# Kernel optimization log

Measured on AMD Instinct MI355X. Metric: run time of the kernel, lower is better.

## Reference

```python
import jax, jax.numpy as jnp
import numpy as np

T_SEQ = 120
BATCH = 256
HID = 512
D_LAG = 32
D_COV = 32
D_OUT = 1
N_LAYERS = 2
D_IN0 = D_LAG + D_COV
BN_EPS = 1e-5
SCALE_EPS = 1e-6
GAMMA = 1.0


def _gru_layer(x, Wih, Whh, bih, bhh):
    # x: [B, T, D] -> [B, T, H]; PyTorch GRU gate order (r, z, n)
    H = Whh.shape[1]
    gx = jnp.einsum('btd,gd->btg', x, Wih) + bih  # [B, T, 3H]
    gx_t = jnp.swapaxes(gx, 0, 1)                 # [T, B, 3H]
    h0 = jnp.zeros((x.shape[0], H), x.dtype)

    def step(h, g):
        gh = h @ Whh.T + bhh
        r = jax.nn.sigmoid(g[:, :H] + gh[:, :H])
        z = jax.nn.sigmoid(g[:, H:2 * H] + gh[:, H:2 * H])
        n = jnp.tanh(g[:, 2 * H:] + r * gh[:, 2 * H:])
        h = (1.0 - z) * n + z * h
        return h, h

    _, hs = jax.lax.scan(step, h0, gx_t)
    return jnp.swapaxes(hs, 0, 1)  # [B, T, H]


def setup_inputs() -> dict:
    key = jax.random.key(0)
    ks = jax.random.split(key, 16)
    s = 1.0 / np.sqrt(HID)
    inp = {
        'X_emb': jnp.zeros((T_SEQ, BATCH, 1), dtype=jnp.int32),
        'X_cov': jax.random.normal(ks[0], (T_SEQ, BATCH, D_COV), dtype=jnp.float32),
        'X_lag': jax.random.normal(ks[1], (T_SEQ, BATCH, D_LAG), dtype=jnp.float32),
        'y': jax.random.normal(ks[2], (T_SEQ, BATCH, D_OUT), dtype=jnp.float32),
        'd_outputseqlen': 24,
        'len_win': 30,
        'W_ih0': jax.random.uniform(ks[3], (3 * HID, D_IN0), minval=-s, maxval=s),
        'W_hh0': jax.random.uniform(ks[4], (3 * HID, HID), minval=-s, maxval=s),
        'b_ih0': jax.random.uniform(ks[5], (3 * HID,), minval=-s, maxval=s),
        'b_hh0': jax.random.uniform(ks[6], (3 * HID,), minval=-s, maxval=s),
        'W_ih1': jax.random.uniform(ks[7], (3 * HID, HID), minval=-s, maxval=s),
        'W_hh1': jax.random.uniform(ks[8], (3 * HID, HID), minval=-s, maxval=s),
        'b_ih1': jax.random.uniform(ks[9], (3 * HID,), minval=-s, maxval=s),
        'b_hh1': jax.random.uniform(ks[10], (3 * HID,), minval=-s, maxval=s),
        'gate_W': jax.random.normal(ks[11], (N_LAYERS, T_SEQ, T_SEQ * 2 * HID)) * 0.05,
        'gate_b': jnp.zeros((N_LAYERS, T_SEQ)),
        'bn_gamma': jnp.ones((N_LAYERS, T_SEQ)),
        'bn_beta': jnp.zeros((N_LAYERS, T_SEQ)),
        'fc_W': jax.random.uniform(ks[12], (D_OUT, HID), minval=-s, maxval=s),
        'fc_b': jnp.zeros((D_OUT,)),
    }
    return inp


def reference(X_emb, X_cov, X_lag, y, d_outputseqlen, len_win,
              W_ih0, W_hh0, b_ih0, b_hh0, W_ih1, W_hh1, b_ih1, b_hh1,
              gate_W, gate_b, bn_gamma, bn_beta, fc_W, fc_b):
    T, B, _ = X_lag.shape
    half = B // 2
    x = jnp.concatenate([X_lag, X_cov], axis=-1)   # [T, B, D]
    x = jnp.transpose(x, (1, 0, 2))                # [B, T, D]

    gru_params = [(W_ih0, W_hh0, b_ih0, b_hh0), (W_ih1, W_hh1, b_ih1, b_hh1)]
    outs = []
    gate_weights = []
    for l, (Wih, Whh, bih, bhh) in enumerate(gru_params):
        x = _gru_layer(x, Wih, Whh, bih, bhh)      # [B, T, H]
        outs.append(x)
        # process_gate_weight: src/tgt halves concatenated on feature dim
        x_all = jnp.concatenate([x[:half], x[half:]], axis=2).reshape(half, -1)  # [B/2, T*2H]
        z = x_all @ gate_W[l].T + gate_b[l]        # [B/2, T]
        m = z.mean(axis=0)
        v = ((z - m) ** 2).mean(axis=0)            # biased var (BatchNorm training mode)
        w = jax.nn.sigmoid(bn_gamma[l] * (z - m) / jnp.sqrt(v + BN_EPS) + bn_beta[l])
        gate_weights.append(jax.nn.softmax(w.mean(axis=0)))  # [T]

    # prediction head (original uses fc_scale for both loc and scale)
    fea = outs[-1]
    lin = fea[:, -d_outputseqlen:, :] @ fc_W.T + fc_b          # [B, L, D_OUT]
    y_hat_loc = jnp.transpose(lin, (1, 0, 2))                  # [L, B, D_OUT]
    y_hat_scale = jnp.transpose(jax.nn.softplus(lin), (1, 0, 2)) + SCALE_EPS
    y_t = y[-d_outputseqlen:]
    log_prob = (-0.5 * ((y_t - y_hat_loc) / y_hat_scale) ** 2
                - jnp.log(y_hat_scale) - 0.5 * jnp.log(2.0 * jnp.pi))
    loss_y = -log_prob.mean()

    # linear-MMD transfer loss over windowed (j, k) pairs, all layers
    idx = jnp.arange(T)
    mask = (jnp.abs(idx[:, None] - idx[None, :]) <= len_win).astype(fea.dtype)  # [T, T]
    loss_transfer = jnp.zeros(())
    for l, o in enumerate(outs):
        ms = o[:half].mean(axis=0)   # [T, H]
        mt = o[half:].mean(axis=0)   # [T, H]
        # D[j,k] = ||ms[j]-mt[k]||^2 == linear MMD of columns j (src) and k (tgt)
        D = ((ms ** 2).sum(-1)[:, None] + (mt ** 2).sum(-1)[None, :]
             - 2.0 * ms @ mt.T)
        loss_transfer = loss_transfer + jnp.dot(gate_weights[l], (mask * D).sum(axis=1))
    total_loss = loss_y + GAMMA * loss_transfer
    return (total_loss, loss_y, y_hat_loc, y_hat_scale, jnp.stack(gate_weights))
```

## Files before the change

kernel.cpp:

```cpp
#include <hip/hip_runtime.h>
#include <math.h>

#define T_SEQ 120
#define BATCH 256
#define HID   512
#define G3    1536
#define MROWS (BATCH*T_SEQ)
#define TS    (T_SEQ*HID)
#define KGATE 122880
#define FSTRIDE 16

typedef __attribute__((ext_vector_type(8))) short bf16x8;
typedef __attribute__((ext_vector_type(4))) float f32x4;

__device__ __forceinline__ unsigned short f2bf(float f) {
    union { float f; unsigned u; } x; x.f = f;
    unsigned r = x.u + 0x7fffu + ((x.u >> 16) & 1u);
    return (unsigned short)(r >> 16);
}
__device__ __forceinline__ float bf2f(unsigned short u) {
    union { unsigned u; float f; } x; x.u = ((unsigned)u) << 16; return x.f;
}
__device__ __forceinline__ float sigm_fast(float x) {
    return 1.f / (1.f + __expf(-x));
}
__device__ __forceinline__ float tanh_fast(float x) {
    float e = __expf(2.f * x);
    return 1.f - 2.f / (e + 1.f);
}

__global__ void build_x(const float* __restrict__ X_lag,
                        const float* __restrict__ X_cov,
                        float* __restrict__ x_in)
{
    int idx = blockIdx.x * 256 + threadIdx.x;
    int d = idx & 63;
    int m = idx >> 6;
    int b = m / 120, t = m - b * 120;
    float v;
    if (d < 32) v = X_lag[((size_t)t * BATCH + b) * 32 + d];
    else        v = X_cov[((size_t)t * BATCH + b) * 32 + (d - 32)];
    x_in[idx] = v;
}

__global__ void cast_whh0(const float* __restrict__ W, unsigned short* __restrict__ o)
{
    int i = blockIdx.x * 256 + threadIdx.x;
    o[i] = f2bf(W[i]);
}

__global__ void cast_wcat1(const float* __restrict__ Whh, const float* __restrict__ Wih,
                           unsigned short* __restrict__ o)
{
    int i = blockIdx.x * 256 + threadIdx.x;
    int row = i >> 10, c = i & 1023;
    float v = (c < 512) ? Whh[row * 512 + c] : Wih[row * 512 + (c - 512)];
    o[i] = f2bf(v);
}

__global__ void mkbias(const float* __restrict__ bih0, const float* __restrict__ bhh0,
                       const float* __restrict__ bih1, const float* __restrict__ bhh1,
                       float* __restrict__ bcomb0, float* __restrict__ bc1)
{
    int n = blockIdx.x * 256 + threadIdx.x;
    bcomb0[n] = bih0[n] + (n < 1024 ? bhh0[n] : 0.f);
    bc1[n]    = bih1[n] + (n < 1024 ? bhh1[n] : 0.f);
}

__global__ __launch_bounds__(256) void gemm_abt_t(
    const float* __restrict__ A, const float* __restrict__ B,
    const float* __restrict__ bias, unsigned short* __restrict__ C,
    int M, int N, int K)
{
    __shared__ float As[32][129];
    __shared__ float Bs[32][129];
    int m0 = blockIdx.x * 128;
    int n0 = blockIdx.y * 128;
    int tid = threadIdx.x;
    int tx = tid & 15, ty = tid >> 4;
    float acc[8][8] = {};
    for (int k0 = 0; k0 < K; k0 += 32) {
        #pragma unroll
        for (int i = 0; i < 16; i++) {
            int e = tid + i * 256;
            int row = e >> 5, col = e & 31;
            As[col][row] = A[(size_t)(m0 + row) * K + k0 + col];
            Bs[col][row] = B[(size_t)(n0 + row) * K + k0 + col];
        }
        __syncthreads();
        #pragma unroll
        for (int kk = 0; kk < 32; kk++) {
            float a[8], b[8];
            #pragma unroll
            for (int i = 0; i < 8; i++) a[i] = As[kk][ty + i * 16];
            #pragma unroll
            for (int j = 0; j < 8; j++) b[j] = Bs[kk][tx + j * 16];
            #pragma unroll
            for (int i = 0; i < 8; i++)
                #pragma unroll
                for (int j = 0; j < 8; j++) acc[i][j] += a[i] * b[j];
        }
        __syncthreads();
    }
    #pragma unroll
    for (int i = 0; i < 8; i++) {
        int m = m0 + ty + i * 16;
        int b = m / 120, t = m - b * 120;
        #pragma unroll
        for (int j = 0; j < 8; j++) {
            int n = n0 + tx + j * 16;
            C[((size_t)t * 256 + b) * G3 + n] = f2bf(acc[i][j] + bias[n]);
        }
    }
}

__device__ __forceinline__ bool wait16(const int* __restrict__ fb, int thr, int lane)
{
    const int* ap = fb + (lane & 15) * FSTRIDE;
    for (int it = 0; it < 100000; ++it) {
        int v = __hip_atomic_load(ap, __ATOMIC_RELAXED, __HIP_MEMORY_SCOPE_AGENT);
        if (__all(v >= thr)) return true;
        __builtin_amdgcn_s_sleep(1);
    }
    return false;
}

__global__ __launch_bounds__(256) void gru_xcd(
    const unsigned short* __restrict__ gx0,
    const unsigned short* __restrict__ Whh0,
    const unsigned short* __restrict__ Wcat1,
    const float* __restrict__ bhh0,
    const float* __restrict__ bc1,
    const float* __restrict__ bhh1,
    unsigned short* __restrict__ out0,
    unsigned short* __restrict__ out1,
    int* __restrict__ flags,
    int* __restrict__ rolecnt)
{
    __shared__ unsigned short wlds[96 * 520];
    __shared__ int role_s;

    int xcd;
    asm("s_getreg_b32 %0, hwreg(20, 0, 32)" : "=s"(xcd));
    xcd &= 7;
    if (threadIdx.x == 0) role_s = atomicAdd(&rolecnt[xcd * 16], 1);
    __syncthreads();
    const int role = role_s;
    if (role >= 32) return;

    const int layer = role >> 4;
    const int jb    = role & 15;
    const int j0    = jb * 32;
    const int tid   = threadIdx.x;
    const int w     = tid >> 6, lane = tid & 63;
    const int l15   = lane & 15, l4 = lane >> 4;
    const int jt    = w & 1, bt = w >> 1;
    const int jloc  = jt * 16 + l15;
    const int j     = j0 + jloc;
    const int bloc0 = bt * 16;
    const int bg0   = xcd * 32;

    {
        const unsigned short* Wsrc = layer ? Wcat1 : Whh0;
        const int wstr = layer ? 1024 : 512;
        for (int c = tid; c < 96 * 64; c += 256) {
            int lr = c >> 6, ck = c & 63;
            int grow = (lr >> 5) * 512 + j0 + (lr & 31);
            bf16x8 v = *(const bf16x8*)(Wsrc + (size_t)grow * wstr + ck * 8);
            *(bf16x8*)&wlds[lr * 520 + ck * 8] = v;
        }
    }
    float bn_, br_ = 0.f, bz_ = 0.f, bnx_ = 0.f;
    if (layer) { br_ = bc1[j]; bz_ = bc1[512 + j]; bnx_ = bc1[1024 + j]; bn_ = bhh1[1024 + j]; }
    else       { bn_ = bhh0[1024 + j]; }
    float carry[4] = {0.f, 0.f, 0.f, 0.f};

    const int* f0b = flags + (0 * 8 + xcd) * 16 * FSTRIDE;
    const int* f1b = flags + (1 * 8 + xcd) * 16 * FSTRIDE;
    int* myf = flags + ((layer * 8 + xcd) * 16 + jb) * FSTRIDE;
    __syncthreads();

    if (!layer) {
        for (int t = 0; t < T_SEQ; t++) {
            unsigned short gr_[4], gz_[4], gn_[4];
            #pragma unroll
            for (int rr = 0; rr < 4; rr++) {
                int b = bg0 + bloc0 + 4 * l4 + rr;
                const unsigned short* gp = gx0 + ((size_t)t * 256 + b) * G3 + j;
                gr_[rr] = gp[0]; gz_[rr] = gp[512]; gn_[rr] = gp[1024];
            }
            asm volatile("" ::: "memory");

            if (!wait16(f0b, t - 1, lane)) break;

            f32x4 a0 = {0,0,0,0}, a1 = {0,0,0,0}, a2 = {0,0,0,0};
            if (t > 0) {
                bf16x8 Areg[16];
                #pragma unroll
                for (int ks = 0; ks < 16; ks++)
                    Areg[ks] = *(const bf16x8*)(out0 + ((size_t)(bg0 + bloc0 + l15) * T_SEQ + (t - 1)) * 512 + ks * 32 + 8 * l4);
                #pragma unroll
                for (int ks = 0; ks < 16; ks++) {
                    const int ko = ks * 32 + 8 * l4;
                    bf16x8 B0 = *(const bf16x8*)&wlds[(0 * 32 + jloc) * 520 + ko];
                    bf16x8 B1 = *(const bf16x8*)&wlds[(1 * 32 + jloc) * 520 + ko];
                    bf16x8 B2 = *(const bf16x8*)&wlds[(2 * 32 + jloc) * 520 + ko];
                    a0 = __builtin_amdgcn_mfma_f32_16x16x32_bf16(Areg[ks], B0, a0, 0, 0, 0);
                    a1 = __builtin_amdgcn_mfma_f32_16x16x32_bf16(Areg[ks], B1, a1, 0, 0, 0);
                    a2 = __builtin_amdgcn_mfma_f32_16x16x32_bf16(Areg[ks], B2, a2, 0, 0, 0);
                }
            }
            #pragma unroll
            for (int rr = 0; rr < 4; rr++) {
                int b = bg0 + bloc0 + 4 * l4 + rr;
                float r = sigm_fast(bf2f(gr_[rr]) + a0[rr]);
                float z = sigm_fast(bf2f(gz_[rr]) + a1[rr]);
                float n = tanh_fast(bf2f(gn_[rr]) + r * (a2[rr] + bn_));
                float h = (1.f - z) * n + z * carry[rr];
                carry[rr] = h;
                out0[((size_t)b * T_SEQ + t) * 512 + j] = f2bf(h);
            }
            asm volatile("s_waitcnt vmcnt(0)" ::: "memory");
            __syncthreads();
            if (tid == 0)
                __hip_atomic_store(myf, t, __ATOMIC_RELAXED, __HIP_MEMORY_SCOPE_AGENT);
        }
    } else {
        for (int t = 0; t < T_SEQ; t++) {
            f32x4 a0 = {0,0,0,0}, a1 = {0,0,0,0}, a2 = {0,0,0,0}, a3 = {0,0,0,0};
            if (!wait16(f1b, t - 1, lane)) break;
            if (t > 0) {
                bf16x8 Areg[16];
                #pragma unroll
                for (int ks = 0; ks < 16; ks++)
                    Areg[ks] = *(const bf16x8*)(out1 + ((size_t)(bg0 + bloc0 + l15) * T_SEQ + (t - 1)) * 512 + ks * 32 + 8 * l4);
                #pragma unroll
                for (int ks = 0; ks < 16; ks++) {
                    const int ko = ks * 32 + 8 * l4;
                    bf16x8 B0 = *(const bf16x8*)&wlds[(0 * 32 + jloc) * 520 + ko];
                    bf16x8 B1 = *(const bf16x8*)&wlds[(1 * 32 + jloc) * 520 + ko];
                    bf16x8 B2 = *(const bf16x8*)&wlds[(2 * 32 + jloc) * 520 + ko];
                    a0 = __builtin_amdgcn_mfma_f32_16x16x32_bf16(Areg[ks], B0, a0, 0, 0, 0);
                    a1 = __builtin_amdgcn_mfma_f32_16x16x32_bf16(Areg[ks], B1, a1, 0, 0, 0);
                    a2 = __builtin_amdgcn_mfma_f32_16x16x32_bf16(Areg[ks], B2, a2, 0, 0, 0);
                }
            }
            if (!wait16(f0b, t, lane)) break;
            {
                bf16x8 Areg[16];
                #pragma unroll
                for (int ks = 0; ks < 16; ks++)
                    Areg[ks] = *(const bf16x8*)(out0 + ((size_t)(bg0 + bloc0 + l15) * T_SEQ + t) * 512 + ks * 32 + 8 * l4);
                #pragma unroll
                for (int ks = 0; ks < 16; ks++) {
                    const int ko = ks * 32 + 8 * l4;
                    const unsigned short* wb = Wcat1 + (size_t)j * 1024 + 512 + ko;
                    bf16x8 B0 = *(const bf16x8*)(wb);
                    bf16x8 B1 = *(const bf16x8*)(wb + 512 * 1024);
                    bf16x8 B2 = *(const bf16x8*)(wb + 1024 * 1024);
                    a0 = __builtin_amdgcn_mfma_f32_16x16x32_bf16(Areg[ks], B0, a0, 0, 0, 0);
                    a1 = __builtin_amdgcn_mfma_f32_16x16x32_bf16(Areg[ks], B1, a1, 0, 0, 0);
                    a3 = __builtin_amdgcn_mfma_f32_16x16x32_bf16(Areg[ks], B2, a3, 0, 0, 0);
                }
            }
            #pragma unroll
            for (int rr = 0; rr < 4; rr++) {
                int b = bg0 + bloc0 + 4 * l4 + rr;
                float r = sigm_fast(a0[rr] + br_);
                float z = sigm_fast(a1[rr] + bz_);
                float n = tanh_fast(a3[rr] + bnx_ + r * (a2[rr] + bn_));
                float h = (1.f - z) * n + z * carry[rr];
                carry[rr] = h;
                out1[((size_t)b * T_SEQ + t) * 512 + j] = f2bf(h);
            }
            asm volatile("s_waitcnt vmcnt(0)" ::: "memory");
            __syncthreads();
            if (tid == 0)
                __hip_atomic_store(myf, t, __ATOMIC_RELAXED, __HIP_MEMORY_SCOPE_AGENT);
        }
    }
}

__global__ __launch_bounds__(256) void zpart_kernel(
    const unsigned short* __restrict__ out, const float* __restrict__ Gw,
    float* __restrict__ zp)
{
    __shared__ float Os[128][33];
    __shared__ float Gs[128][33];
    int bk = blockIdx.x;
    int t = bk >> 3, half = (bk >> 2) & 1, cq = bk & 3;
    int tid = threadIdx.x;
    int tx = tid & 15, ty = tid >> 4;
    float acc[8][8] = {};
    int cbase = cq * 128;
    for (int c0 = cbase; c0 < cbase + 128; c0 += 32) {
        #pragma unroll
        for (int i = 0; i < 16; i++) {
            int e = tid + i * 256;
            int row = e >> 5, col = e & 31;
            Os[row][col] = bf2f(out[((size_t)(row + half * 128) * T_SEQ + t) * 512 + c0 + col]);
            float v = 0.f;
            if (row < 120)
                v = Gw[(size_t)row * KGATE + (size_t)t * 1024 + half * 512 + c0 + col];
            Gs[row][col] = v;
        }
        __syncthreads();
        #pragma unroll
        for (int kk = 0; kk < 32; kk++) {
            float a[8], g[8];
            #pragma unroll
            for (int i = 0; i < 8; i++) a[i] = Os[ty + i * 16][kk];
            #pragma unroll
            for (int j = 0; j < 8; j++) g[j] = Gs[tx + j * 16][kk];
            #pragma unroll
            for (int i = 0; i < 8; i++)
                #pragma unroll
                for (int j = 0; j < 8; j++) acc[i][j] += a[i] * g[j];
        }
        __syncthreads();
    }
    float* zb = zp + (size_t)bk * (128 * 120);
    #pragma unroll
    for (int i = 0; i < 8; i++) {
        int ii = ty + i * 16;
        #pragma unroll
        for (int j = 0; j < 8; j++) {
            int r = tx + j * 16;
            if (r < 120) zb[ii * 120 + r] = acc[i][j];
        }
    }
}

__global__ void zreduce(const float* __restrict__ zp,
                        const float* __restrict__ gate_b_l,
                        float* __restrict__ z)
{
    int idx = blockIdx.x * 256 + threadIdx.x;
    if (idx >= 128 * 120) return;
    float s = 0.f;
    for (int c = 0; c < 960; c++) s += zp[(size_t)c * (128 * 120) + idx];
    z[idx] = s + gate_b_l[idx % 120];
}

__global__ __launch_bounds__(128) void bn_col(
    const float* __restrict__ z, const float* __restrict__ gamma,
    const float* __restrict__ beta, float* __restrict__ wm)
{
    int r = blockIdx.x, i = threadIdx.x;
    __shared__ float sh[2];
    float v = z[i * 120 + r];
    float s = v;
    for (int o = 32; o > 0; o >>= 1) s += __shfl_down(s, o);
    if ((i & 63) == 0) sh[i >> 6] = s;
    __syncthreads();
    float m = (sh[0] + sh[1]) * (1.f / 128.f);
    __syncthreads();
    float d = (v - m) * (v - m);
    for (int o = 32; o > 0; o >>= 1) d += __shfl_down(d, o);
    if ((i & 63) == 0) sh[i >> 6] = d;
    __syncthreads();
    float var = (sh[0] + sh[1]) * (1.f / 128.f);
    float w = 1.f / (1.f + expf(-(gamma[r] * (v - m) / sqrtf(var + 1e-5f) + beta[r])));
    __syncthreads();
    float ws_ = w;
    for (int o = 32; o > 0; o >>= 1) ws_ += __shfl_down(ws_, o);
    if ((i & 63) == 0) sh[i >> 6] = ws_;
    __syncthreads();
    if (i == 0) wm[r] = (sh[0] + sh[1]) * (1.f / 128.f);
}

__global__ __launch_bounds__(128) void softmax120(
    const float* __restrict__ wm, float* __restrict__ g_out,
    float* __restrict__ g_ws)
{
    int i = threadIdx.x;
    __shared__ float sh[2];
    float v = (i < 120) ? wm[i] : -1e30f;
    float m = v;
    for (int o = 32; o > 0; o >>= 1) m = fmaxf(m, __shfl_down(m, o));
    if ((i & 63) == 0) sh[i >> 6] = m;
    __syncthreads();
    float mx = fmaxf(sh[0], sh[1]);
    float e = (i < 120) ? expf(v - mx) : 0.f;
    __syncthreads();
    float se = e;
    for (int o = 32; o > 0; o >>= 1) se += __shfl_down(se, o);
    if ((i & 63) == 0) sh[i >> 6] = se;
    __syncthreads();
    float sum = sh[0] + sh[1];
    if (i < 120) { float g = e / sum; g_out[i] = g; g_ws[i] = g; }
}

__global__ void halfmeans(const unsigned short* __restrict__ out,
                          float* __restrict__ ms, float* __restrict__ mt)
{
    int idx = blockIdx.x * 256 + threadIdx.x;
    int half = idx >= TS;
    int tc = idx - half * TS;
    const unsigned short* base = out + (size_t)(half * 128) * TS + tc;
    float s = 0.f;
    for (int i = 0; i < 128; i++) s += bf2f(base[(size_t)i * TS]);
    s *= (1.f / 128.f);
    if (half) mt[tc] = s; else ms[tc] = s;
}

__global__ __launch_bounds__(512) void transfer_part(
    const float* __restrict__ ms, const float* __restrict__ mt,
    const float* __restrict__ gw, const int* __restrict__ lenw,
    float* __restrict__ part)
{
    int t = blockIdx.x, c = threadIdx.x;
    int lw = lenw[0];
    int j0 = t - lw; if (j0 < 0) j0 = 0;
    int j1 = t + lw; if (j1 > 119) j1 = 119;
    float m_c = ms[(size_t)t * 512 + c];
    float acc = 0.f;
    for (int j = j0; j <= j1; j++) {
        float d = m_c - mt[(size_t)j * 512 + c];
        acc += d * d;
    }
    for (int o = 32; o > 0; o >>= 1) acc += __shfl_down(acc, o);
    __shared__ float sh[8];
    if ((c & 63) == 0) sh[c >> 6] = acc;
    __syncthreads();
    if (c == 0) {
        float s = 0.f;
        #pragma unroll
        for (int k = 0; k < 8; k++) s += sh[k];
        part[t] = gw[t] * s;
    }
}

__global__ __launch_bounds__(256) void yhat_kernel(
    const unsigned short* __restrict__ out1, const float* __restrict__ y,
    const float* __restrict__ fcW, const float* __restrict__ fcb,
    int dsl, float* __restrict__ dout, float* __restrict__ lp_rows)
{
    int wid = blockIdx.x * 4 + (threadIdx.x >> 6);
    int lane = threadIdx.x & 63;
    int tt = wid >> 8, b = wid & 255;
    int t = T_SEQ - dsl + tt;
    const unsigned short* row = out1 + ((size_t)b * T_SEQ + t) * 512;
    float s = 0.f;
    #pragma unroll
    for (int k = 0; k < 8; k++) s += bf2f(row[lane + 64 * k]) * fcW[lane + 64 * k];
    for (int o = 32; o > 0; o >>= 1) s += __shfl_down(s, o);
    if (lane == 0) {
        float loc = s + fcb[0];
        float sp = fmaxf(loc, 0.f) + log1pf(expf(-fabsf(loc)));
        float scale = sp + 1e-6f;
        dout[2 + tt * 256 + b] = loc;
        dout[2 + dsl * 256 + tt * 256 + b] = scale;
        float yt = y[(size_t)t * 256 + b];
        float u = (yt - loc) / scale;
        lp_rows[wid] = -0.5f * u * u - logf(scale) - 0.91893853320467274f;
    }
}

__global__ __launch_bounds__(64) void finalize(
    const float* __restrict__ lp_rows, const float* __restrict__ part0,
    const float* __restrict__ part1, float* __restrict__ dout, int n_lp)
{
    int i = threadIdx.x;
    float s = 0.f;
    for (int k = i; k < n_lp; k += 64) s += lp_rows[k];
    for (int o = 32; o > 0; o >>= 1) s += __shfl_down(s, o);
    float tr = 0.f;
    for (int k = i; k < 120; k += 64) tr += part0[k] + part1[k];
    for (int o = 32; o > 0; o >>= 1) tr += __shfl_down(tr, o);
    if (i == 0) {
        float ly = -s / (float)n_lp;
        dout[1] = ly;
        dout[0] = ly + tr;
    }
}

extern "C" void kernel_launch(void* const* d_in, const int* in_sizes, int n_in,
                              void* d_out, int out_size, void* d_ws, size_t ws_size,
                              hipStream_t stream)
{
    const float* X_cov  = (const float*)d_in[1];
    const float* X_lag  = (const float*)d_in[2];
    const float* y      = (const float*)d_in[3];
    const int*   lenw   = (const int*)d_in[5];
    const float* W_ih0  = (const float*)d_in[6];
    const float* W_hh0  = (const float*)d_in[7];
    const float* b_ih0  = (const float*)d_in[8];
    const float* b_hh0  = (const float*)d_in[9];
    const float* W_ih1  = (const float*)d_in[10];
    const float* W_hh1  = (const float*)d_in[11];
    const float* b_ih1  = (const float*)d_in[12];
    const float* b_hh1  = (const float*)d_in[13];
    const float* gate_W = (const float*)d_in[14];
    const float* gate_b = (const float*)d_in[15];
    const float* bn_g   = (const float*)d_in[16];
    const float* bn_b   = (const float*)d_in[17];
    const float* fc_W   = (const float*)d_in[18];
    const float* fc_b   = (const float*)d_in[19];
    float* dout = (float*)d_out;
    float* ws   = (float*)d_ws;

    float* x_in    = ws;
    unsigned short* gx0bf = (unsigned short*)(ws + 1966080);
    unsigned short* out0  = (unsigned short*)(ws + 25559040);
    unsigned short* out1  = (unsigned short*)(ws + 33423360);
    unsigned short* Whh0bf  = (unsigned short*)(ws + 41287680);
    unsigned short* Wcat1bf = (unsigned short*)(ws + 41680896);
    float* zmat    = ws + 42467328;
    float* wm      = ws + 42482688;
    float* gw_ws   = ws + 42482808;
    float* msb     = ws + 42483048;
    float* mtb     = ws + 42544488;
    float* part    = ws + 42605928;
    float* bcomb0  = ws + 42606168;
    float* bc1     = ws + 42607704;
    int*   flags   = (int*)(ws + 42609240);
    int*   rolecnt = (int*)(ws + 42613336);
    float* zp      = ws + 1966080;
    float* lp_rows = x_in;

    int dsl = (out_size - 2 - 2 * T_SEQ) / (2 * BATCH);

    build_x<<<dim3(7680), 256, 0, stream>>>(X_lag, X_cov, x_in);
    cast_whh0<<<dim3(3072), 256, 0, stream>>>(W_hh0, Whh0bf);
    cast_wcat1<<<dim3(6144), 256, 0, stream>>>(W_hh1, W_ih1, Wcat1bf);
    mkbias<<<dim3(6), 256, 0, stream>>>(b_ih0, b_hh0, b_ih1, b_hh1, bcomb0, bc1);
    hipMemsetAsync(flags, 0xFF, 4096 * sizeof(int), stream);
    hipMemsetAsync(rolecnt, 0, 128 * sizeof(int), stream);

    gemm_abt_t<<<dim3(240, 12), 256, 0, stream>>>(x_in, W_ih0, bcomb0, gx0bf,
                                                  MROWS, G3, 64);

    gru_xcd<<<dim3(320), 256, 0, stream>>>(gx0bf, Whh0bf, Wcat1bf,
                                           b_hh0, bc1, b_hh1,
                                           out0, out1, flags, rolecnt);

    for (int l = 0; l < 2; l++) {
        const unsigned short* o = l ? out1 : out0;
        zpart_kernel<<<960, 256, 0, stream>>>(o, gate_W + (size_t)l * 120 * KGATE, zp);
        zreduce<<<60, 256, 0, stream>>>(zp, gate_b + l * 120, zmat);
        bn_col<<<120, 128, 0, stream>>>(zmat, bn_g + l * 120, bn_b + l * 120, wm);
        softmax120<<<1, 128, 0, stream>>>(wm, dout + 2 + 2 * dsl * 256 + l * 120,
                                          gw_ws + l * 120);
        halfmeans<<<480, 256, 0, stream>>>(o, msb, mtb);
        transfer_part<<<120, 512, 0, stream>>>(msb, mtb, gw_ws + l * 120, lenw,
                                               part + l * 120);
    }

    yhat_kernel<<<dsl * 64, 256, 0, stream>>>(out1, y, fc_W, fc_b, dsl, dout, lp_rows);
    finalize<<<1, 64, 0, stream>>>(lp_rows, part, part + 120, dout, dsl * 256);
}
```

Measured before the change: 1.893 ms.

## Replace per-block flag barriers with per-wave atomic step counters in GRU

The per-block flag array, where each block waits on 16 flags with a block-wide __syncthreads before publishing, is replaced by one shared counter per layer and XCD. Each wave increments it after its stores and spins on it reaching 64*t. This removes the intra-block barrier and the 16-way flag poll, and waves proceed independently. In exchange, 64 waves contend on a single atomic cache line and the spin has no sleep, which may add memory traffic. Wave-level fetch_add after only a vmcnt wait could also weaken ordering.

```diff
diff --git a/kernel.cpp b/kernel.cpp
--- a/kernel.cpp
+++ b/kernel.cpp
@@ -8,7 +8,7 @@
 #define MROWS (BATCH*T_SEQ)
 #define TS    (T_SEQ*HID)
 #define KGATE 122880
-#define FSTRIDE 16
+#define CSTRIDE 32
 
 typedef __attribute__((ext_vector_type(8))) short bf16x8;
 typedef __attribute__((ext_vector_type(4))) float f32x4;
@@ -114,13 +114,11 @@
     }
 }
 
-__device__ __forceinline__ bool wait16(const int* __restrict__ fb, int thr, int lane)
-{
-    const int* ap = fb + (lane & 15) * FSTRIDE;
-    for (int it = 0; it < 100000; ++it) {
-        int v = __hip_atomic_load(ap, __ATOMIC_RELAXED, __HIP_MEMORY_SCOPE_AGENT);
-        if (__all(v >= thr)) return true;
-        __builtin_amdgcn_s_sleep(1);
+__device__ __forceinline__ bool wave_wait(const int* __restrict__ cnt, int thr)
+{
+    for (int it = 0; it < 2000000; ++it) {
+        int v = __hip_atomic_load(cnt, __ATOMIC_RELAXED, __HIP_MEMORY_SCOPE_AGENT);
+        if (v >= thr) return true;
     }
     return false;
 }
@@ -134,7 +132,7 @@
     const float* __restrict__ bhh1,
     unsigned short* __restrict__ out0,
     unsigned short* __restrict__ out1,
-    int* __restrict__ flags,
+    int* __restrict__ cnts,
     int* __restrict__ rolecnt)
 {
     __shared__ unsigned short wlds[96 * 520];
@@ -175,9 +173,9 @@
     else       { bn_ = bhh0[1024 + j]; }
     float carry[4] = {0.f, 0.f, 0.f, 0.f};
 
-    const int* f0b = flags + (0 * 8 + xcd) * 16 * FSTRIDE;
-    const int* f1b = flags + (1 * 8 + xcd) * 16 * FSTRIDE;
-    int* myf = flags + ((layer * 8 + xcd) * 16 + jb) * FSTRIDE;
+    const int* c0 = cnts + (0 * 8 + xcd) * CSTRIDE;
+    const int* c1 = cnts + (1 * 8 + xcd) * CSTRIDE;
+    int* myc = cnts + ((layer * 8 + xcd)) * CSTRIDE;
     __syncthreads();
 
     if (!layer) {
@@ -191,7 +189,7 @@
             }
             asm volatile("" ::: "memory");
 
-            if (!wait16(f0b, t - 1, lane)) break;
+            if (!wave_wait(c0, 64 * t)) break;
 
             f32x4 a0 = {0,0,0,0}, a1 = {0,0,0,0}, a2 = {0,0,0,0};
             if (t > 0) {
@@ -221,14 +219,14 @@
                 out0[((size_t)b * T_SEQ + t) * 512 + j] = f2bf(h);
             }
             asm volatile("s_waitcnt vmcnt(0)" ::: "memory");
-            __syncthreads();
-            if (tid == 0)
-                __hip_atomic_store(myf, t, __ATOMIC_RELAXED, __HIP_MEMORY_SCOPE_AGENT);
+            if (lane == 0)
+                __hip_atomic_fetch_add(myc, 1, __ATOMIC_RELAXED,
+                                       __HIP_MEMORY_SCOPE_AGENT);
         }
     } else {
         for (int t = 0; t < T_SEQ; t++) {
             f32x4 a0 = {0,0,0,0}, a1 = {0,0,0,0}, a2 = {0,0,0,0}, a3 = {0,0,0,0};
-            if (!wait16(f1b, t - 1, lane)) break;
+            if (!wave_wait(c1, 64 * t)) break;
             if (t > 0) {
                 bf16x8 Areg[16];
                 #pragma unroll
@@ -245,7 +243,7 @@
                     a2 = __builtin_amdgcn_mfma_f32_16x16x32_bf16(Areg[ks], B2, a2, 0, 0, 0);
                 }
             }
-            if (!wait16(f0b, t, lane)) break;
+            if (!wave_wait(c0, 64 * (t + 1))) break;
             {
                 bf16x8 Areg[16];
                 #pragma unroll
@@ -274,9 +272,9 @@
                 out1[((size_t)b * T_SEQ + t) * 512 + j] = f2bf(h);
             }
             asm volatile("s_waitcnt vmcnt(0)" ::: "memory");
-            __syncthreads();
-            if (tid == 0)
-                __hip_atomic_store(myf, t, __ATOMIC_RELAXED, __HIP_MEMORY_SCOPE_AGENT);
+            if (lane == 0)
+                __hip_atomic_fetch_add(myc, 1, __ATOMIC_RELAXED,
+                                       __HIP_MEMORY_SCOPE_AGENT);
         }
     }
 }
@@ -514,7 +512,7 @@
     float* part    = ws + 42605928;
     float* bcomb0  = ws + 42606168;
     float* bc1     = ws + 42607704;
-    int*   flags   = (int*)(ws + 42609240);
+    int*   cnts    = (int*)(ws + 42609240);
     int*   rolecnt = (int*)(ws + 42613336);
     float* zp      = ws + 1966080;
     float* lp_rows = x_in;
@@ -525,7 +523,7 @@
     cast_whh0<<<dim3(3072), 256, 0, stream>>>(W_hh0, Whh0bf);
     cast_wcat1<<<dim3(6144), 256, 0, stream>>>(W_hh1, W_ih1, Wcat1bf);
     mkbias<<<dim3(6), 256, 0, stream>>>(b_ih0, b_hh0, b_ih1, b_hh1, bcomb0, bc1);
-    hipMemsetAsync(flags, 0xFF, 4096 * sizeof(int), stream);
+    hipMemsetAsync(cnts, 0, 16 * CSTRIDE * sizeof(int), stream);
     hipMemsetAsync(rolecnt, 0, 128 * sizeof(int), stream);
 
     gemm_abt_t<<<dim3(240, 12), 256, 0, stream>>>(x_in, W_ih0, bcomb0, gx0bf,
@@ -533,7 +531,7 @@
 
     gru_xcd<<<dim3(320), 256, 0, stream>>>(gx0bf, Whh0bf, Wcat1bf,
                                            b_hh0, bc1, b_hh1,
-                                           out0, out1, flags, rolecnt);
+                                           out0, out1, cnts, rolecnt);
 
     for (int l = 0; l < 2; l++) {
         const unsigned short* o = l ? out1 : out0;
```

After: 2.083 ms. 10.0% more time.

## Switch GRU step sync to per-wave flags and drop block barriers

Applied to the files above, without the earlier changes.

Each wavefront now publishes its own progress flag, so every group tracks 64 flags instead of 16. This removes the __syncthreads before each flag store, and each lane polls one flag. Spin-waits no longer sleep, and layer 1 checks both of its dependencies in a single combined poll instead of two sequential waits. The flag buffer and memset grow to match, and rolecnt moves to a new offset. The intent is lower per-timestep synchronisation latency in the sequential recurrence, at the cost of more polling traffic and busy-spinning.

```diff
diff --git a/kernel.cpp b/kernel.cpp
--- a/kernel.cpp
+++ b/kernel.cpp
@@ -114,13 +114,28 @@
     }
 }
 
-__device__ __forceinline__ bool wait16(const int* __restrict__ fb, int thr, int lane)
-{
-    const int* ap = fb + (lane & 15) * FSTRIDE;
-    for (int it = 0; it < 100000; ++it) {
+__device__ __forceinline__ bool wait64(const int* __restrict__ base, int thr,
+                                       int lane)
+{
+    const int* ap = base + lane * FSTRIDE;
+    for (int it = 0; it < 2000000; ++it) {
         int v = __hip_atomic_load(ap, __ATOMIC_RELAXED, __HIP_MEMORY_SCOPE_AGENT);
         if (__all(v >= thr)) return true;
-        __builtin_amdgcn_s_sleep(1);
+    }
+    return false;
+}
+__device__ __forceinline__ bool wait64x2(const int* __restrict__ b0, int thr0,
+                                         const int* __restrict__ b1, int thr1,
+                                         int lane)
+{
+    const int* a0 = b0 + lane * FSTRIDE;
+    const int* a1 = b1 + lane * FSTRIDE;
+    for (int it = 0; it < 2000000; ++it) {
+        int v0 = __hip_atomic_load(a0, __ATOMIC_RELAXED, __HIP_MEMORY_SCOPE_AGENT);
+        int v1 = __hip_atomic_load(a1, __ATOMIC_RELAXED, __HIP_MEMORY_SCOPE_AGENT);
+        bool ok0 = __all(v0 >= thr0);
+        bool ok1 = __all(v1 >= thr1);
+        if (ok0 && ok1) return true;
     }
     return false;
 }
@@ -175,9 +190,9 @@
     else       { bn_ = bhh0[1024 + j]; }
     float carry[4] = {0.f, 0.f, 0.f, 0.f};
 
-    const int* f0b = flags + (0 * 8 + xcd) * 16 * FSTRIDE;
-    const int* f1b = flags + (1 * 8 + xcd) * 16 * FSTRIDE;
-    int* myf = flags + ((layer * 8 + xcd) * 16 + jb) * FSTRIDE;
+    const int* f0b = flags + (0 * 8 + xcd) * 64 * FSTRIDE;
+    const int* f1b = flags + (1 * 8 + xcd) * 64 * FSTRIDE;
+    int* myf = flags + ((layer * 8 + xcd) * 64 + (jb * 4 + w)) * FSTRIDE;
     __syncthreads();
 
     if (!layer) {
@@ -191,7 +206,7 @@
             }
             asm volatile("" ::: "memory");
 
-            if (!wait16(f0b, t - 1, lane)) break;
+            if (!wait64(f0b, t - 1, lane)) break;
 
             f32x4 a0 = {0,0,0,0}, a1 = {0,0,0,0}, a2 = {0,0,0,0};
             if (t > 0) {
@@ -221,14 +236,14 @@
                 out0[((size_t)b * T_SEQ + t) * 512 + j] = f2bf(h);
             }
             asm volatile("s_waitcnt vmcnt(0)" ::: "memory");
-            __syncthreads();
-            if (tid == 0)
+            if (lane == 0)
                 __hip_atomic_store(myf, t, __ATOMIC_RELAXED, __HIP_MEMORY_SCOPE_AGENT);
         }
     } else {
         for (int t = 0; t < T_SEQ; t++) {
+            if (!wait64x2(f1b, t - 1, f0b, t, lane)) break;
+
             f32x4 a0 = {0,0,0,0}, a1 = {0,0,0,0}, a2 = {0,0,0,0}, a3 = {0,0,0,0};
-            if (!wait16(f1b, t - 1, lane)) break;
             if (t > 0) {
                 bf16x8 Areg[16];
                 #pragma unroll
@@ -245,7 +260,6 @@
                     a2 = __builtin_amdgcn_mfma_f32_16x16x32_bf16(Areg[ks], B2, a2, 0, 0, 0);
                 }
             }
-            if (!wait16(f0b, t, lane)) break;
             {
                 bf16x8 Areg[16];
                 #pragma unroll
@@ -274,8 +288,7 @@
                 out1[((size_t)b * T_SEQ + t) * 512 + j] = f2bf(h);
             }
             asm volatile("s_waitcnt vmcnt(0)" ::: "memory");
-            __syncthreads();
-            if (tid == 0)
+            if (lane == 0)
                 __hip_atomic_store(myf, t, __ATOMIC_RELAXED, __HIP_MEMORY_SCOPE_AGENT);
         }
     }
@@ -515,7 +528,7 @@
     float* bcomb0  = ws + 42606168;
     float* bc1     = ws + 42607704;
     int*   flags   = (int*)(ws + 42609240);
-    int*   rolecnt = (int*)(ws + 42613336);
+    int*   rolecnt = (int*)(ws + 42625624);
     float* zp      = ws + 1966080;
     float* lp_rows = x_in;
 
@@ -525,7 +538,7 @@
     cast_whh0<<<dim3(3072), 256, 0, stream>>>(W_hh0, Whh0bf);
     cast_wcat1<<<dim3(6144), 256, 0, stream>>>(W_hh1, W_ih1, Wcat1bf);
     mkbias<<<dim3(6), 256, 0, stream>>>(b_ih0, b_hh0, b_ih1, b_hh1, bcomb0, bc1);
-    hipMemsetAsync(flags, 0xFF, 4096 * sizeof(int), stream);
+    hipMemsetAsync(flags, 0xFF, 16384 * sizeof(int), stream);
     hipMemsetAsync(rolecnt, 0, 128 * sizeof(int), stream);
 
     gemm_abt_t<<<dim3(240, 12), 256, 0, stream>>>(x_in, W_ih0, bcomb0, gx0bf,
```

Result: slower. 2.058 ms (+8.7%).

## Fuse layer-0 input projection into GRU kernel and busy-spin flag waits

Applied to the files above, without the earlier changes.

Drops the build_x and layer-0 input GEMM kernels. Layer-0 GRU blocks now load their W_ih0 slice into LDS and compute the input gate contributions per timestep from X_lag/X_cov in fp32, before waiting on the previous step's flag, which removes the gx0 bf16 intermediate round-trip. The flag wait loop replaces s_sleep with dummy FMA work so polling reacts faster, and zreduce's serial sum is split into 8 independent accumulators. The trade-off is extra per-step FMA work and global X loads inside the recurrent critical path, plus busier spinning that competes for issue slots.

```diff
diff --git a/kernel.cpp b/kernel.cpp
--- a/kernel.cpp
+++ b/kernel.cpp
@@ -5,7 +5,6 @@
 #define BATCH 256
 #define HID   512
 #define G3    1536
-#define MROWS (BATCH*T_SEQ)
 #define TS    (T_SEQ*HID)
 #define KGATE 122880
 #define FSTRIDE 16
@@ -29,20 +28,6 @@
     return 1.f - 2.f / (e + 1.f);
 }
 
-__global__ void build_x(const float* __restrict__ X_lag,
-                        const float* __restrict__ X_cov,
-                        float* __restrict__ x_in)
-{
-    int idx = blockIdx.x * 256 + threadIdx.x;
-    int d = idx & 63;
-    int m = idx >> 6;
-    int b = m / 120, t = m - b * 120;
-    float v;
-    if (d < 32) v = X_lag[((size_t)t * BATCH + b) * 32 + d];
-    else        v = X_cov[((size_t)t * BATCH + b) * 32 + (d - 32)];
-    x_in[idx] = v;
-}
-
 __global__ void cast_whh0(const float* __restrict__ W, unsigned short* __restrict__ o)
 {
     int i = blockIdx.x * 256 + threadIdx.x;
@@ -67,69 +52,36 @@
     bc1[n]    = bih1[n] + (n < 1024 ? bhh1[n] : 0.f);
 }
 
-__global__ __launch_bounds__(256) void gemm_abt_t(
-    const float* __restrict__ A, const float* __restrict__ B,
-    const float* __restrict__ bias, unsigned short* __restrict__ C,
-    int M, int N, int K)
-{
-    __shared__ float As[32][129];
-    __shared__ float Bs[32][129];
-    int m0 = blockIdx.x * 128;
-    int n0 = blockIdx.y * 128;
-    int tid = threadIdx.x;
-    int tx = tid & 15, ty = tid >> 4;
-    float acc[8][8] = {};
-    for (int k0 = 0; k0 < K; k0 += 32) {
+__device__ __forceinline__ bool wait16(const int* __restrict__ fb, int thr, int lane)
+{
+    const int* ap = fb + (lane & 15) * FSTRIDE;
+    float x0 = (float)lane, x1 = x0 + 1.f, x2 = x0 + 2.f, x3 = x0 + 3.f;
+    for (int it = 0; it < 300000; ++it) {
+        int v = __hip_atomic_load(ap, __ATOMIC_RELAXED, __HIP_MEMORY_SCOPE_AGENT);
+        if (__all(v >= thr)) {
+            asm volatile("" :: "v"(x0), "v"(x1), "v"(x2), "v"(x3));
+            return true;
+        }
         #pragma unroll
-        for (int i = 0; i < 16; i++) {
-            int e = tid + i * 256;
-            int row = e >> 5, col = e & 31;
-            As[col][row] = A[(size_t)(m0 + row) * K + k0 + col];
-            Bs[col][row] = B[(size_t)(n0 + row) * K + k0 + col];
-        }
-        __syncthreads();
-        #pragma unroll
-        for (int kk = 0; kk < 32; kk++) {
-            float a[8], b[8];
-            #pragma unroll
-            for (int i = 0; i < 8; i++) a[i] = As[kk][ty + i * 16];
-            #pragma unroll
-            for (int j = 0; j < 8; j++) b[j] = Bs[kk][tx + j * 16];
-            #pragma unroll
-            for (int i = 0; i < 8; i++)
-                #pragma unroll
-                for (int j = 0; j < 8; j++) acc[i][j] += a[i] * b[j];
-        }
-        __syncthreads();
-    }
-    #pragma unroll
-    for (int i = 0; i < 8; i++) {
-        int m = m0 + ty + i * 16;
-        int b = m / 120, t = m - b * 120;
-        #pragma unroll
-        for (int j = 0; j < 8; j++) {
-            int n = n0 + tx + j * 16;
-            C[((size_t)t * 256 + b) * G3 + n] = f2bf(acc[i][j] + bias[n]);
-        }
-    }
-}
-
-__device__ __forceinline__ bool wait16(const int* __restrict__ fb, int thr, int lane)
-{
-    const int* ap = fb + (lane & 15) * FSTRIDE;
-    for (int it = 0; it < 100000; ++it) {
-        int v = __hip_atomic_load(ap, __ATOMIC_RELAXED, __HIP_MEMORY_SCOPE_AGENT);
-        if (__all(v >= thr)) return true;
-        __builtin_amdgcn_s_sleep(1);
-    }
+        for (int q = 0; q < 12; q++) {
+            x0 = __builtin_fmaf(x0, 1.000001f, 1e-7f);
+            x1 = __builtin_fmaf(x1, 1.000001f, 1e-7f);
+            x2 = __builtin_fmaf(x2, 1.000001f, 1e-7f);
+            x3 = __builtin_fmaf(x3, 1.000001f, 1e-7f);
+        }
+    }
+    asm volatile("" :: "v"(x0), "v"(x1), "v"(x2), "v"(x3));
     return false;
 }
 
 __global__ __launch_bounds__(256) void gru_xcd(
-    const unsigned short* __restrict__ gx0,
+    const float* __restrict__ X_lag,
+    const float* __restrict__ X_cov,
+    const float* __restrict__ Wih0,
     const unsigned short* __restrict__ Whh0,
     const unsigned short* __restrict__ Wcat1,
     const float* __restrict__ bhh0,
+    const float* __restrict__ bcomb0,
     const float* __restrict__ bc1,
     const float* __restrict__ bhh1,
     unsigned short* __restrict__ out0,
@@ -138,6 +90,7 @@
     int* __restrict__ rolecnt)
 {
     __shared__ unsigned short wlds[96 * 520];
+    __shared__ float wih[96 * 68];
     __shared__ int role_s;
 
     int xcd;
@@ -170,9 +123,17 @@
             *(bf16x8*)&wlds[lr * 520 + ck * 8] = v;
         }
     }
+    if (!layer) {
+        for (int c = tid; c < 96 * 16; c += 256) {
+            int row = c >> 4, q = c & 15;
+            int grow = (row >> 5) * 512 + j0 + (row & 31);
+            float4 v = *(const float4*)(Wih0 + (size_t)grow * 64 + q * 4);
+            *(float4*)&wih[row * 68 + q * 4] = v;
+        }
+    }
     float bn_, br_ = 0.f, bz_ = 0.f, bnx_ = 0.f;
     if (layer) { br_ = bc1[j]; bz_ = bc1[512 + j]; bnx_ = bc1[1024 + j]; bn_ = bhh1[1024 + j]; }
-    else       { bn_ = bhh0[1024 + j]; }
+    else       { br_ = bcomb0[j]; bz_ = bcomb0[512 + j]; bnx_ = bcomb0[1024 + j]; bn_ = bhh0[1024 + j]; }
     float carry[4] = {0.f, 0.f, 0.f, 0.f};
 
     const int* f0b = flags + (0 * 8 + xcd) * 16 * FSTRIDE;
@@ -182,14 +143,24 @@
 
     if (!layer) {
         for (int t = 0; t < T_SEQ; t++) {
-            unsigned short gr_[4], gz_[4], gn_[4];
+            float dr[4] = {}, dz[4] = {}, dn[4] = {};
             #pragma unroll
-            for (int rr = 0; rr < 4; rr++) {
-                int b = bg0 + bloc0 + 4 * l4 + rr;
-                const unsigned short* gp = gx0 + ((size_t)t * 256 + b) * G3 + j;
-                gr_[rr] = gp[0]; gz_[rr] = gp[512]; gn_[rr] = gp[1024];
+            for (int kc = 0; kc < 16; kc++) {
+                float4 w0 = *(const float4*)&wih[(0 * 32 + jloc) * 68 + kc * 4];
+                float4 w1 = *(const float4*)&wih[(1 * 32 + jloc) * 68 + kc * 4];
+                float4 w2 = *(const float4*)&wih[(2 * 32 + jloc) * 68 + kc * 4];
+                #pragma unroll
+                for (int rr = 0; rr < 4; rr++) {
+                    int b = bg0 + bloc0 + 4 * l4 + rr;
+                    const float* xr = (kc < 8)
+                        ? X_lag + ((size_t)t * 256 + b) * 32 + kc * 4
+                        : X_cov + ((size_t)t * 256 + b) * 32 + (kc - 8) * 4;
+                    float4 xv = *(const float4*)xr;
+                    dr[rr] += xv.x * w0.x + xv.y * w0.y + xv.z * w0.z + xv.w * w0.w;
+                    dz[rr] += xv.x * w1.x + xv.y * w1.y + xv.z * w1.z + xv.w * w1.w;
+                    dn[rr] += xv.x * w2.x + xv.y * w2.y + xv.z * w2.z + xv.w * w2.w;
+                }
             }
-            asm volatile("" ::: "memory");
 
             if (!wait16(f0b, t - 1, lane)) break;
 
@@ -213,9 +184,9 @@
             #pragma unroll
             for (int rr = 0; rr < 4; rr++) {
                 int b = bg0 + bloc0 + 4 * l4 + rr;
-                float r = sigm_fast(bf2f(gr_[rr]) + a0[rr]);
-                float z = sigm_fast(bf2f(gz_[rr]) + a1[rr]);
-                float n = tanh_fast(bf2f(gn_[rr]) + r * (a2[rr] + bn_));
+                float r = sigm_fast(dr[rr] + br_ + a0[rr]);
+                float z = sigm_fast(dz[rr] + bz_ + a1[rr]);
+                float n = tanh_fast(dn[rr] + bnx_ + r * (a2[rr] + bn_));
                 float h = (1.f - z) * n + z * carry[rr];
                 carry[rr] = h;
                 out0[((size_t)b * T_SEQ + t) * 512 + j] = f2bf(h);
@@ -337,9 +308,19 @@
 {
     int idx = blockIdx.x * 256 + threadIdx.x;
     if (idx >= 128 * 120) return;
-    float s = 0.f;
-    for (int c = 0; c < 960; c++) s += zp[(size_t)c * (128 * 120) + idx];
-    z[idx] = s + gate_b_l[idx % 120];
+    const float* p = zp + idx;
+    float s0 = 0, s1 = 0, s2 = 0, s3 = 0, s4 = 0, s5 = 0, s6 = 0, s7 = 0;
+    for (int c = 0; c < 960; c += 8) {
+        s0 += p[(size_t)(c + 0) * 15360];
+        s1 += p[(size_t)(c + 1) * 15360];
+        s2 += p[(size_t)(c + 2) * 15360];
+        s3 += p[(size_t)(c + 3) * 15360];
+        s4 += p[(size_t)(c + 4) * 15360];
+        s5 += p[(size_t)(c + 5) * 15360];
+        s6 += p[(size_t)(c + 6) * 15360];
+        s7 += p[(size_t)(c + 7) * 15360];
+    }
+    z[idx] = ((s0 + s1) + (s2 + s3)) + ((s4 + s5) + (s6 + s7)) + gate_b_l[idx % 120];
 }
 
 __global__ __launch_bounds__(128) void bn_col(
@@ -500,39 +481,34 @@
     float* dout = (float*)d_out;
     float* ws   = (float*)d_ws;
 
-    float* x_in    = ws;
-    unsigned short* gx0bf = (unsigned short*)(ws + 1966080);
-    unsigned short* out0  = (unsigned short*)(ws + 25559040);
-    unsigned short* out1  = (unsigned short*)(ws + 33423360);
-    unsigned short* Whh0bf  = (unsigned short*)(ws + 41287680);
-    unsigned short* Wcat1bf = (unsigned short*)(ws + 41680896);
-    float* zmat    = ws + 42467328;
-    float* wm      = ws + 42482688;
-    float* gw_ws   = ws + 42482808;
-    float* msb     = ws + 42483048;
-    float* mtb     = ws + 42544488;
-    float* part    = ws + 42605928;
-    float* bcomb0  = ws + 42606168;
-    float* bc1     = ws + 42607704;
-    int*   flags   = (int*)(ws + 42609240);
-    int*   rolecnt = (int*)(ws + 42613336);
-    float* zp      = ws + 1966080;
-    float* lp_rows = x_in;
+    unsigned short* out0  = (unsigned short*)(ws);
+    unsigned short* out1  = (unsigned short*)(ws + 7864320);
+    unsigned short* Whh0bf  = (unsigned short*)(ws + 15728640);
+    unsigned short* Wcat1bf = (unsigned short*)(ws + 16121856);
+    float* zp      = ws + 16908288;
+    float* zmat    = ws + 31653888;
+    float* wm      = ws + 31669248;
+    float* gw_ws   = ws + 31669368;
+    float* msb     = ws + 31669608;
+    float* mtb     = ws + 31731048;
+    float* part    = ws + 31792488;
+    float* bcomb0  = ws + 31792728;
+    float* bc1     = ws + 31794264;
+    int*   flags   = (int*)(ws + 31795800);
+    int*   rolecnt = (int*)(ws + 31799896);
+    float* lp_rows = ws + 31800024;
 
     int dsl = (out_size - 2 - 2 * T_SEQ) / (2 * BATCH);
 
-    build_x<<<dim3(7680), 256, 0, stream>>>(X_lag, X_cov, x_in);
     cast_whh0<<<dim3(3072), 256, 0, stream>>>(W_hh0, Whh0bf);
     cast_wcat1<<<dim3(6144), 256, 0, stream>>>(W_hh1, W_ih1, Wcat1bf);
     mkbias<<<dim3(6), 256, 0, stream>>>(b_ih0, b_hh0, b_ih1, b_hh1, bcomb0, bc1);
     hipMemsetAsync(flags, 0xFF, 4096 * sizeof(int), stream);
     hipMemsetAsync(rolecnt, 0, 128 * sizeof(int), stream);
 
-    gemm_abt_t<<<dim3(240, 12), 256, 0, stream>>>(x_in, W_ih0, bcomb0, gx0bf,
-                                                  MROWS, G3, 64);
-
-    gru_xcd<<<dim3(320), 256, 0, stream>>>(gx0bf, Whh0bf, Wcat1bf,
-                                           b_hh0, bc1, b_hh1,
+    gru_xcd<<<dim3(320), 256, 0, stream>>>(X_lag, X_cov, W_ih0,
+                                           Whh0bf, Wcat1bf,
+                                           b_hh0, bcomb0, bc1, b_hh1,
                                            out0, out1, flags, rolecnt);
 
     for (int l = 0; l < 2; l++) {
```

Result: faster. 1.839 ms (-2.9%).
